# Optimization experiments

Measured on AMD Instinct MI355X. Metric: run time of the kernel, lower is better.

The kernel has to match this reference:

```python
import math
import jax, jax.numpy as jnp
from jax import lax
import numpy as np

N_IMG = 2
C = 128
IMG_H, IMG_W = 512, 1024
STRIDES = (4, 8, 16, 32, 64)
SIZES = (32.0, 64.0, 128.0, 256.0, 512.0)
RATIOS = (0.5, 1.0, 2.0)
A = len(RATIOS)
PRE_NMS_TOPK = 2000    # pre_nms_topk[self.training] with training=True
POST_NMS_TOPK = 1000   # post_nms_topk[self.training]
NMS_THRESH = 0.7
BATCH_PER_IMG = 256
POS_FRAC = 0.5
MIN_BOX_SIZE = 0.0
SCALE_CLAMP = math.log(1000.0 / 16.0)
MATCH_LOW, MATCH_HIGH = 0.3, 0.7


def cell_anchors(size):
    rs = jnp.asarray(RATIOS, jnp.float32)
    area = size * size
    w = jnp.sqrt(area / rs)
    h = w * rs
    return jnp.stack([-w / 2, -h / 2, w / 2, h / 2], axis=1)  # [A,4]


def level_anchors(H, W, stride, size):
    ca = cell_anchors(size)
    sx = jnp.arange(W, dtype=jnp.float32) * stride
    sy = jnp.arange(H, dtype=jnp.float32) * stride
    yy, xx = jnp.meshgrid(sy, sx, indexing="ij")
    shifts = jnp.stack([xx, yy, xx, yy], axis=-1).reshape(-1, 4)  # [H*W,4]
    return (shifts[:, None, :] + ca[None, :, :]).reshape(-1, 4)  # [H*W*A,4]


def pairwise_iou(a, b):
    lt = jnp.maximum(a[:, None, :2], b[None, :, :2])
    rb = jnp.minimum(a[:, None, 2:], b[None, :, 2:])
    wh = jnp.clip(rb - lt, 0.0)
    inter = wh[..., 0] * wh[..., 1]
    area_a = (a[:, 2] - a[:, 0]) * (a[:, 3] - a[:, 1])
    area_b = (b[:, 2] - b[:, 0]) * (b[:, 3] - b[:, 1])
    union = area_a[:, None] + area_b[None, :] - inter
    return jnp.where(inter > 0, inter / union, 0.0)


def get_deltas(src, tgt):
    sw = src[..., 2] - src[..., 0]; sh = src[..., 3] - src[..., 1]
    scx = src[..., 0] + 0.5 * sw;   scy = src[..., 1] + 0.5 * sh
    tw = tgt[..., 2] - tgt[..., 0]; th = tgt[..., 3] - tgt[..., 1]
    tcx = tgt[..., 0] + 0.5 * tw;   tcy = tgt[..., 1] + 0.5 * th
    return jnp.stack([(tcx - scx) / sw, (tcy - scy) / sh,
                      jnp.log(tw / sw), jnp.log(th / sh)], axis=-1)


def apply_deltas(deltas, boxes):
    w = boxes[..., 2] - boxes[..., 0]; h = boxes[..., 3] - boxes[..., 1]
    cx = boxes[..., 0] + 0.5 * w;      cy = boxes[..., 1] + 0.5 * h
    dx, dy = deltas[..., 0], deltas[..., 1]
    dw = jnp.minimum(deltas[..., 2], SCALE_CLAMP)
    dh = jnp.minimum(deltas[..., 3], SCALE_CLAMP)
    pcx = dx * w + cx; pcy = dy * h + cy
    pw = jnp.exp(dw) * w; ph = jnp.exp(dh) * h
    return jnp.stack([pcx - 0.5 * pw, pcy - 0.5 * ph,
                      pcx + 0.5 * pw, pcy + 0.5 * ph], axis=-1)


def conv(x, w, b):
    y = lax.conv_general_dilated(x, w, (1, 1), "SAME",
                                 dimension_numbers=("NCHW", "OIHW", "NCHW"))
    return y + b[None, :, None, None]


def rpn_forward_flat(feats, conv_w, conv_b, obj_w, obj_b, delta_w, delta_b):
    anchors, logits, deltas = [], [], []
    for (stride, size), f in zip(zip(STRIDES, SIZES), feats):
        N, _, H, W = f.shape
        h = jax.nn.relu(conv(f, conv_w, conv_b))
        lg = conv(h, obj_w, obj_b)       # [N,A,H,W]
        dl = conv(h, delta_w, delta_b)   # [N,4A,H,W]
        logits.append(lg.transpose(0, 2, 3, 1).reshape(N, -1))                     # [N,HWA]
        deltas.append(dl.reshape(N, A, 4, H, W).transpose(0, 3, 4, 1, 2).reshape(N, -1, 4))
        anchors.append(level_anchors(H, W, stride, size))
    return anchors, logits, deltas


def label_and_sample(gt_b, key, anchors_all):
    iou = pairwise_iou(gt_b, anchors_all)                 # [G,R]
    matched_idxs = jnp.argmax(iou, axis=0)
    matched_vals = jnp.max(iou, axis=0)
    labels = jnp.where(matched_vals >= MATCH_HIGH, 1,
             jnp.where(matched_vals >= MATCH_LOW, -1, 0))
    highest = jnp.max(iou, axis=1)                        # per-gt best IoU
    lq = jnp.any((iou == highest[:, None]) & (highest[:, None] > 0), axis=0)
    labels = jnp.where(lq, 1, labels)                     # allow_low_quality_matches
    R = labels.shape[0]
    kf, kb = jax.random.split(key)
    fg = labels == 1; bg = labels == 0
    num_fg = jnp.minimum(fg.sum(), int(POS_FRAC * BATCH_PER_IMG))
    num_bg = jnp.minimum(bg.sum(), BATCH_PER_IMG - num_fg)
    def pick(mask, k, num):
        pri = jnp.where(mask, jax.random.uniform(k, (R,)), jnp.inf)
        rank = jnp.argsort(jnp.argsort(pri))
        return rank < num
    sel_fg = pick(fg, kf, num_fg)
    sel_bg = pick(bg, kb, num_bg)
    labels = jnp.where(sel_fg, 1, jnp.where(sel_bg, 0, -1))
    return labels, gt_b[matched_idxs]


def losses_fn(anchors_all, logits_cat, deltas_cat, gt_labels, matched_gt):
    fg = (gt_labels == 1).astype(logits_cat.dtype)          # [N,R]
    gt_deltas = get_deltas(anchors_all[None], matched_gt)   # [N,R,4]
    loc = jnp.sum(jnp.abs(deltas_cat - gt_deltas) * fg[..., None])  # smooth_l1, beta=0
    valid = (gt_labels >= 0).astype(logits_cat.dtype)
    x = logits_cat
    bce = jnp.maximum(x, 0.0) - x * fg + jnp.log1p(jnp.exp(-jnp.abs(x)))
    cls = jnp.sum(bce * valid)
    norm = float(BATCH_PER_IMG) * logits_cat.shape[0]
    return jnp.stack([cls / norm, loc / norm])


def nms_keep(boxes, valid):
    # boxes are sorted by descending score; greedy suppression.
    K = boxes.shape[0]
    iou = pairwise_iou(boxes, boxes)
    idx = jnp.arange(K)
    def body(i, keep):
        sup = (iou[i] > NMS_THRESH) & (idx > i) & keep[i]
        return keep & ~sup
    return lax.fori_loop(0, K, body, valid)


def predict_proposals(anchors, logits, deltas):
    lvl_boxes, lvl_scores = [], []
    for anc, lg, dl in zip(anchors, logits, deltas):
        boxes = apply_deltas(dl, anc[None])             # [N,R_l,4]
        k = min(PRE_NMS_TOPK, lg.shape[1])
        ts, ti = lax.top_k(lg, k)                       # [N,k]
        tb = jnp.take_along_axis(boxes, ti[..., None], axis=1)
        tb = jnp.stack([jnp.clip(tb[..., 0], 0.0, IMG_W), jnp.clip(tb[..., 1], 0.0, IMG_H),
                        jnp.clip(tb[..., 2], 0.0, IMG_W), jnp.clip(tb[..., 3], 0.0, IMG_H)], -1)
        valid = ((tb[..., 2] - tb[..., 0]) > MIN_BOX_SIZE) & ((tb[..., 3] - tb[..., 1]) > MIN_BOX_SIZE)
        keep = jax.vmap(nms_keep)(tb, valid)
        lvl_boxes.append(tb)
        lvl_scores.append(jnp.where(keep, ts, -jnp.inf))
    all_b = jnp.concatenate(lvl_boxes, axis=1)
    all_s = jnp.concatenate(lvl_scores, axis=1)
    fs, fi = lax.top_k(all_s, POST_NMS_TOPK)
    fb = jnp.take_along_axis(all_b, fi[..., None], axis=1)
    return fb, fs


def setup_inputs() -> dict:
    key = jax.random.key(0)
    ks = jax.random.split(key, 12)
    out = {}
    for i, s in enumerate(STRIDES):
        out[f"feat_p{i+2}"] = jax.random.normal(ks[i], (N_IMG, C, IMG_H // s, IMG_W // s), jnp.float32)
    G = 32
    wh_scale = jnp.asarray([IMG_W, IMG_H], jnp.float32)
    cxy = jax.random.uniform(ks[5], (N_IMG, G, 2)) * wh_scale
    wh = 32.0 + jax.random.uniform(ks[6], (N_IMG, G, 2)) * 224.0
    x1y1 = jnp.clip(cxy - wh / 2, 0.0)
    x2y2 = jnp.maximum(jnp.minimum(cxy + wh / 2, wh_scale), x1y1 + 1.0)
    out["gt_boxes"] = jnp.concatenate([x1y1, x2y2], axis=-1)
    out["conv_w"] = 0.01 * jax.random.normal(ks[7], (C, C, 3, 3), jnp.float32)
    out["conv_b"] = jnp.zeros((C,), jnp.float32)
    out["obj_w"] = 0.01 * jax.random.normal(ks[8], (A, C, 1, 1), jnp.float32)
    out["obj_b"] = jnp.zeros((A,), jnp.float32)
    out["delta_w"] = 0.01 * jax.random.normal(ks[9], (4 * A, C, 1, 1), jnp.float32)
    out["delta_b"] = jnp.zeros((4 * A,), jnp.float32)
    return out


def reference(feat_p2, feat_p3, feat_p4, feat_p5, feat_p6, gt_boxes,
              conv_w, conv_b, obj_w, obj_b, delta_w, delta_b):
    feats = [feat_p2, feat_p3, feat_p4, feat_p5, feat_p6]
    anchors, logits, deltas = rpn_forward_flat(feats, conv_w, conv_b, obj_w, obj_b, delta_w, delta_b)
    anchors_all = jnp.concatenate(anchors, axis=0)      # [R,4]
    logits_cat = jnp.concatenate(logits, axis=1)        # [N,R]
    deltas_cat = jnp.concatenate(deltas, axis=1)        # [N,R,4]
    keys = jax.random.split(jax.random.key(42), gt_boxes.shape[0])
    gt_labels, matched_gt = jax.vmap(label_and_sample, in_axes=(0, 0, None))(gt_boxes, keys, anchors_all)
    losses = losses_fn(anchors_all, logits_cat, deltas_cat, gt_labels, matched_gt)
    prop_boxes, prop_scores = predict_proposals(
        anchors,
        [lax.stop_gradient(l) for l in logits],
        [lax.stop_gradient(d) for d in deltas])
    return prop_boxes, prop_scores, losses
```

## Files before the change

kernel.cpp:

```cpp
#include <hip/hip_runtime.h>
#include <stdint.h>
#include <math.h>


#define R_TOT   130944
#define HALF_R  65472
#define TOTK    7920
#define SCALE_CLAMP 4.135166556742356

__host__ __device__ inline void threefry(uint32_t k0, uint32_t k1,
                                         uint32_t x0, uint32_t x1,
                                         uint32_t* o0, uint32_t* o1)
{
  uint32_t ks[3]; ks[0]=k0; ks[1]=k1; ks[2]=k0^k1^0x1BD11BDAu;
  x0 += ks[0]; x1 += ks[1];
  const uint32_t rot0[4] = {13u,15u,26u,6u};
  const uint32_t rot1[4] = {17u,29u,16u,24u};
  for (int i = 0; i < 5; i++){
    const uint32_t* rot = (i & 1) ? rot1 : rot0;
    for (int q = 0; q < 4; q++){
      x0 += x1;
      x1 = (x1 << rot[q]) | (x1 >> (32u - rot[q]));
      x1 ^= x0;
    }
    x0 += ks[(i+1)%3];
    x1 += ks[(i+2)%3] + (uint32_t)(i+1);
  }
  *o0 = x0; *o1 = x1;
}

__device__ inline unsigned long long mono64(double v){
  unsigned long long b = (unsigned long long)__double_as_longlong(v);
  return (b & 0x8000000000000000ull) ? ~b : (b | 0x8000000000000000ull);
}

__device__ __forceinline__ double iou_cf(double g0,double g1,double g2,double g3,
                                         double a0,double a1,double a2,double a3){
  #pragma clang fp contract(off)
  double lt0 = fmax(g0,a0), lt1 = fmax(g1,a1);
  double rb0 = fmin(g2,a2), rb1 = fmin(g3,a3);
  double w = rb0-lt0; if (w<0.0) w=0.0;
  double h = rb1-lt1; if (h<0.0) h=0.0;
  double inter = w*h;
  double aa = (g2-g0)*(g3-g1);
  double ab = (a2-a0)*(a3-a1);
  double uni = aa+ab-inter;
  return inter>0.0 ? inter/uni : 0.0;
}

__device__ __forceinline__ void anchor_of(int r, double* o){
  #pragma clang fp contract(off)
  const int    base[5]={0,98304,122880,129024,130560};
  const int    Wl[5]  ={256,128,64,32,16};
  const double strd[5]={4.0,8.0,16.0,32.0,64.0};
  const double size[5]={32.0,64.0,128.0,256.0,512.0};
  const double ratio[3]={0.5,1.0,2.0};
  int l=0; while (l<4 && r>=base[l+1]) l++;
  int rr=r-base[l]; int pix=rr/3; int a=rr-pix*3;
  int x=pix%Wl[l], y=pix/Wl[l];
  double w=sqrt(size[l]*size[l]/ratio[a]);
  double h=w*ratio[a];
  double sx=(double)x*strd[l], sy=(double)y*strd[l];
  o[0]=sx-0.5*w; o[1]=sy-0.5*h; o[2]=sx+0.5*w; o[3]=sy+0.5*h;
}

__device__ __forceinline__ void decode_box(int ridx, const double* __restrict__ d,
                                           double* __restrict__ o){
  double a[4]; anchor_of(ridx,a);
  double w=a[2]-a[0], h=a[3]-a[1];
  double cx=a[0]+0.5*w, cy=a[1]+0.5*h;
  double dw=fmin(d[2],SCALE_CLAMP), dh=fmin(d[3],SCALE_CLAMP);
  double pcx=d[0]*w+cx, pcy=d[1]*h+cy;
  double pw=exp(dw)*w, ph=exp(dh)*h;
  double x1=pcx-0.5*pw, y1=pcy-0.5*ph;
  double x2=pcx+0.5*pw, y2=pcy+0.5*ph;
  o[0]=fmin(fmax(x1,0.0),1024.0); o[1]=fmin(fmax(y1,0.0),512.0);
  o[2]=fmin(fmax(x2,0.0),1024.0); o[3]=fmin(fmax(y2,0.0),512.0);
}

__device__ inline void bitonic_desc(double* sv, int* si, int M, int tid, int nthr){
  for (int k=2;k<=M;k<<=1)
    for (int j=k>>1;j>0;j>>=1){
      __syncthreads();
      for (int i=tid;i<M;i+=nthr){
        int ixj=i^j;
        if (ixj>i){
          double va=sv[i], vb=sv[ixj]; int ia=si[i], ib=si[ixj];
          bool before = (va>vb) || (va==vb && ia<ib);
          bool up = ((i&k)==0);
          if (up ? !before : before){ sv[i]=vb; sv[ixj]=va; si[i]=ib; si[ixj]=ia; }
        }
      }
    }
  __syncthreads();
}

__device__ inline void bitonic_asc_u(uint32_t* sk, int* si, int M, int tid, int nthr){
  for (int k=2;k<=M;k<<=1)
    for (int j=k>>1;j>0;j>>=1){
      __syncthreads();
      for (int i=tid;i<M;i+=nthr){
        int ixj=i^j;
        if (ixj>i){
          uint32_t ka=sk[i], kb=sk[ixj]; int ia=si[i], ib=si[ixj];
          bool before = (ka<kb) || (ka==kb && ia<ib);
          bool up = ((i&k)==0);
          if (up ? !before : before){ sk[i]=kb; sk[ixj]=ka; si[i]=ib; si[ixj]=ia; }
        }
      }
    }
  __syncthreads();
}

__device__ inline void hist_select(int* hist, int kneed, int tid,
                                   int* shb, int* shk){
  for (int off=1; off<256; off<<=1){
    int v=0;
    if (tid<256 && tid>=off) v=hist[tid-off];
    __syncthreads();
    if (tid<256) hist[tid]+=v;
    __syncthreads();
  }
  if (tid<256){
    int prev = tid ? hist[tid-1] : 0;
    if (prev < kneed && kneed <= hist[tid]){ *shb=tid; *shk=kneed-prev; }
    if (tid==255 && kneed > hist[255]){ *shb=255; *shk=kneed-hist[254]; }
  }
  __syncthreads();
}

__global__ __launch_bounds__(256) void k_pre(const float* __restrict__ cw,
    float* __restrict__ cwTf, const float* __restrict__ gt,
    unsigned long long* __restrict__ highest)
{
  const int bx=blockIdx.x, tid=threadIdx.x;
  if (bx < 576){
    int o = bx*256 + tid;
    if (o >= 147456) return;
    int cc = o & 127; int t = o >> 7;
    int k9 = t % 9;  int ci = t / 9;
    cwTf[(size_t)(ci*9+k9)*128 + cc] = cw[(size_t)cc*1152 + ci*9 + k9];
  } else {
    __shared__ double gts[128];
    __shared__ unsigned long long lmax[32];
    const int gb=bx-576;
    const int img=gb>>6, b=gb&63;
    if (tid<128) gts[tid]=(double)gt[img*128+tid];
    if (tid<32) lmax[tid]=0ull;
    __syncthreads();
    double gm[32];
    #pragma unroll
    for (int g=0;g<32;g++) gm[g]=0.0;
    for (int r=b*256+tid; r<R_TOT; r+=64*256){
      double a[4]; anchor_of(r,a);
      #pragma unroll
      for (int g=0;g<32;g++){
        double v=iou_cf(gts[g*4],gts[g*4+1],gts[g*4+2],gts[g*4+3],a[0],a[1],a[2],a[3]);
        gm[g]=fmax(gm[g],v);
      }
    }
    #pragma unroll
    for (int g=0;g<32;g++){
      double v=gm[g];
      #pragma unroll
      for (int off=1; off<64; off<<=1) v=fmax(v,__shfl_xor(v,off));
      if ((tid&63)==0) atomicMax(&lmax[g],(unsigned long long)__double_as_longlong(v));
    }
    __syncthreads();
    if (tid<32) atomicMax(&highest[img*32+tid], lmax[tid]);
  }
}

#define CTH 4
#define CTW 8

__global__ __launch_bounds__(256,3) void k_conv_label(
    const float* __restrict__ f2, const float* __restrict__ f3,
    const float* __restrict__ f4, const float* __restrict__ f5,
    const float* __restrict__ f6,
    const float* __restrict__ cwTf, const float* __restrict__ cb,
    const float* __restrict__ ow, const float* __restrict__ ob,
    const float* __restrict__ dwt, const float* __restrict__ dbt,
    double* __restrict__ logits, double* __restrict__ dpred,
    const float* __restrict__ gt, const unsigned long long* __restrict__ highest,
    int* __restrict__ prelab, int* __restrict__ matched,
    int* __restrict__ labels, int* __restrict__ counts,
    uint32_t* __restrict__ ub,
    uint32_t kf00,uint32_t kf01,uint32_t kb00,uint32_t kb01,
    uint32_t kf10,uint32_t kf11,uint32_t kb10,uint32_t kb11)
{
  __shared__ double fshd[4][6][12];
  __shared__ __align__(16) char ush[18432];
  float*  wshF = (float*)ush;
  double* hshp = (double*)ush;
  __shared__ float hw[15*128];
  __shared__ float hb[15];

  const int tid=threadIdx.x;
  const int vbid = blockIdx.x;

  if (vbid >= 3752){
    int j = (vbid-3752)*256 + tid;
    if (j >= 2*R_TOT) return;
    int slot = j / HALF_R; int t = j - slot*HALF_R;
    uint32_t k0,k1;
    if      (slot==0){k0=kf00;k1=kf01;}
    else if (slot==1){k0=kb00;k1=kb01;}
    else if (slot==2){k0=kf10;k1=kf11;}
    else             {k0=kb10;k1=kb11;}
    uint32_t o0,o1;
    threefry(k0,k1,(uint32_t)t,(uint32_t)(t+HALF_R),&o0,&o1);
    ub[(size_t)slot*R_TOT+t]=o0;
    ub[(size_t)slot*R_TOT+t+HALF_R]=o1;
    return;
  }

  if (vbid >= 2728){
    double* gts=(double*)ush;
    double* hg =(double*)(ush+1024);
    int* wfg=(int*)(ush+1280); int* wbg=(int*)(ush+1296);
    const int lb=vbid-2728;
    const int img=lb>>9, blk=lb&511;
    if (tid<128) gts[tid]=(double)gt[img*128+tid];
    if (tid<32)  hg[tid]=__longlong_as_double((long long)highest[img*32+tid]);
    __syncthreads();
    int r=blk*256+tid;
    const bool ok=(r<R_TOT);
    int lab=-1, bi=0;
    if (ok){
      double a[4]; anchor_of(r,a);
      double best=-1.0; bool lq=false;
      #pragma unroll
      for (int g=0;g<32;g++){
        double v=iou_cf(gts[g*4],gts[g*4+1],gts[g*4+2],gts[g*4+3],a[0],a[1],a[2],a[3]);
        if (v>best){ best=v; bi=g; }
        if (hg[g]>0.0 && v==hg[g]) lq=true;
      }
      lab = lq ? 1 : (best>=0.7 ? 1 : (best>=0.3 ? -1 : 0));
      prelab [(size_t)img*R_TOT+r]=lab;
      matched[(size_t)img*R_TOT+r]=bi;
      labels [(size_t)img*R_TOT+r]=-1;
    }
    unsigned long long bf=__ballot(ok && lab==1);
    unsigned long long bb=__ballot(ok && lab==0);
    const int wid=tid>>6, lane=tid&63;
    if (lane==0){ wfg[wid]=__popcll(bf); wbg[wid]=__popcll(bb); }
    __syncthreads();
    if (tid==0){
      int fcnt=wfg[0]+wfg[1]+wfg[2]+wfg[3];
      int bcnt=wbg[0]+wbg[1]+wbg[2]+wbg[3];
      if (fcnt) atomicAdd(&counts[img*2+0],fcnt);
      if (bcnt) atomicAdd(&counts[img*2+1],bcnt);
    }
    return;
  }

  const int cumt[6]={0,2048,2560,2688,2720,2728};
  const int Hs[5]={128,64,32,16,8}, Wl[5]={256,128,64,32,16};
  const int rbs[5]={0,98304,122880,129024,130560};
  const int lgx[5]={5,4,3,2,1};

  int bid=vbid;
  int lvl=0;
  while (lvl<4 && bid>=cumt[lvl+1]) lvl++;
  int t=bid-cumt[lvl];
  const int img=t&1; const int tt=t>>1;
  const int H=Hs[lvl], W=Wl[lvl], rbase=rbs[lvl];
  const int tx=tt&((1<<lgx[lvl])-1), ty=tt>>lgx[lvl];
  const int x0=tx*CTW, y0=ty*CTH;
  const float* f = lvl==0?f2: lvl==1?f3: lvl==2?f4: lvl==3?f5: f6;

  for (int i=tid;i<15*128;i+=256){
    int o=i>>7, c=i&127;
    hw[i]=(o<3)?ow[o*128+c]:dwt[(o-3)*128+c];
  }
  if (tid<15) hb[tid]=(tid<3)?ob[tid]:dbt[tid-3];

  const int c=tid&127, half=tid>>7;
  double acc[16];
  #pragma unroll
  for (int i=0;i<16;i++) acc[i]=0.0;

  const float* fimg = f + (size_t)img*128*H*W;

  const bool fin_act = (tid < 240);
  int ci_f=0,dy_f=0,dx_f=0; bool fin_valid=false;
  const float* fptr=fimg;
  if (fin_act){
    ci_f=tid/60; int rem=tid-ci_f*60; dy_f=rem/10; dx_f=rem-dy_f*10;
    int y=y0-1+dy_f, x=x0-1+dx_f;
    fin_valid = (y>=0&&y<H&&x>=0&&x<W);
    fptr = fimg + (size_t)ci_f*H*W + (fin_valid ? ((size_t)y*W+x) : 0);
  }
  const size_t fstep=(size_t)4*H*W;
  const float2* wsrc=(const float2*)cwTf;

  float fin_pf=0.f; float2 wpf[9];
  if (fin_act){ fin_pf = fin_valid ? *fptr : 0.f; fptr += fstep; }
  #pragma unroll
  for (int j2=0;j2<9;j2++) wpf[j2]=wsrc[tid+j2*256];

  for (int ci0=0; ci0<128; ci0+=4){
    __syncthreads();
    if (fin_act) fshd[ci_f][dy_f][dx_f]=(double)fin_pf;
    { float2* wdst=(float2*)wshF;
      #pragma unroll
      for (int j2=0;j2<9;j2++) wdst[tid+j2*256]=wpf[j2]; }
    if (ci0+4<128){
      if (fin_act){ fin_pf = fin_valid ? *fptr : 0.f; fptr += fstep; }
      const float2* wn = wsrc + (size_t)(ci0+4)*576;
      #pragma unroll
      for (int j2=0;j2<9;j2++) wpf[j2]=wn[tid+j2*256];
    }
    __syncthreads();
    #pragma unroll
    for (int ci=0;ci<4;ci++){
      double w9d[9];
      #pragma unroll
      for (int k=0;k<9;k++) w9d[k]=(double)wshF[(ci*9+k)*128 + c];
      #pragma unroll
      for (int irl=0;irl<4;irl++){
        int ir=half*2+irl;
        double rowb[10];
        #pragma unroll
        for (int q=0;q<10;q++) rowb[q]=fshd[ci][ir][q];
        #pragma unroll
        for (int orl=0;orl<2;orl++){
          int ky=irl-orl;
          if (ky<0||ky>2) continue;
          #pragma unroll
          for (int px=0;px<8;px++){
            double s=acc[orl*8+px];
            #pragma unroll
            for (int kx=0;kx<3;kx++) s += w9d[ky*3+kx]*rowb[px+kx];
            acc[orl*8+px]=s;
          }
        }
      }
    }
  }
  double bc=(double)cb[c];
  __syncthreads();
  if (half==0){
    #pragma unroll
    for (int pp=0;pp<16;pp++){
      double hv=acc[pp]+bc; if (hv<0.0) hv=0.0;
      hshp[c*17+pp]=hv;
    }
  }
  __syncthreads();
  for (int hp=0;hp<2;hp++){
    if (tid<240){
      int o=tid>>4, p=tid&15;
      double s=(double)hb[o];
      for (int c2=0;c2<128;c2++) s += (double)hw[o*128+c2]*hshp[c2*17+p];
      int pg=hp*16+p;
      int py=pg>>3, px=pg&7;
      int gy=y0+py, gx=x0+px;
      long long pix=(long long)gy*W+gx;
      size_t rb=(size_t)rbase+(size_t)pix*3;
      if (o<3) logits[(size_t)img*R_TOT+rb+o]=s;
      else { int a=(o-3)>>2, jj=(o-3)&3; dpred[((size_t)img*R_TOT+rb+a)*4+jj]=s; }
    }
    if (hp==0){
      __syncthreads();
      if (half==1){
        #pragma unroll
        for (int pp=0;pp<16;pp++){
          double hv=acc[pp]+bc; if (hv<0.0) hv=0.0;
          hshp[c*17+pp]=hv;
        }
      }
      __syncthreads();
    }
  }
}

__global__ __launch_bounds__(1024) void k_mid2(const uint32_t* __restrict__ ub,
    const int* __restrict__ prelab, const int* __restrict__ counts,
    int* __restrict__ labels,
    const double* __restrict__ logits, const double* __restrict__ dpred,
    double* __restrict__ allS, double* __restrict__ allB,
    unsigned long long* __restrict__ keepbuf)
{
  __shared__ __align__(16) char buf[49152];
  __shared__ int hist[256];
  __shared__ int sI0, sI1;
  __shared__ int cnt;
  const int tid=threadIdx.x;

  if (blockIdx.x < 4){
    uint32_t* skey=(uint32_t*)buf; int* sidx=(int*)(buf+16384);
    const int img=blockIdx.x>>1, cls=blockIdx.x&1;
    const int cfg=counts[img*2+0], cbg=counts[img*2+1];
    const int num_fg=cfg<128?cfg:128;
    const int cap_bg=256-num_fg;
    const int num=cls?(cbg<cap_bg?cbg:cap_bg):num_fg;
    if (num<=0) return;
    const int want=cls?0:1;
    const int sel=want;
    const uint32_t* u=ub+(size_t)(img*2+cls)*R_TOT;
    const int* pl=prelab+(size_t)img*R_TOT;
    int* lab=labels+(size_t)img*R_TOT;

    for (int b=tid;b<256;b+=1024) hist[b]=0;
    if (tid==0) cnt=0;
    __syncthreads();
    #pragma unroll 4
    for (int r=tid;r<R_TOT;r+=1024){
      int plr = pl[r];
      uint32_t key = u[r]>>9;
      if (plr==want) atomicAdd(&hist[key>>15],1);
    }
    __syncthreads();
    hist_select(hist, num, tid, &sI0, &sI1);
    const uint32_t bsel=(uint32_t)sI0; const int kneed=sI1;
    #pragma unroll 4
    for (int r=tid;r<R_TOT;r+=1024){
      int plr = pl[r];
      uint32_t key = u[r]>>9;
      if (plr==want){
        uint32_t t8=key>>15;
        if (t8<bsel) lab[r]=sel;
        else if (t8==bsel){ int p=atomicAdd(&cnt,1); if (p<4096){ skey[p]=key; sidx[p]=r; } }
      }
    }
    __syncthreads();
    int n=cnt<4096?cnt:4096;
    for (int i=tid;i<4096;i+=1024) if (i>=n){ skey[i]=0xFFFFFFFFu; sidx[i]=0x7FFFFFFF; }
    bitonic_asc_u(skey,sidx,4096,tid,1024);
    int take = kneed<n?kneed:n;
    for (int i=tid;i<take;i+=1024) lab[sidx[i]]=sel;
  } else {
    double* sv=(double*)buf; int* si=(int*)(buf+32768);
    const int Rl[5]   ={98304,24576,6144,1536,384};
    const int kl[5]   ={2000,2000,2000,1536,384};
    const int lbase[5]={0,98304,122880,129024,130560};
    const int loff[5] ={0,2000,4000,6000,7536};
    const int bb=blockIdx.x-4;
    const int lvl=bb%5, img=bb/5;
    if (lvl==0 && tid<124) keepbuf[img*124+tid]=~0ull;
    const int Rn=Rl[lvl], K=kl[lvl];
    const double* lg=logits+(size_t)img*R_TOT+lbase[lvl];

    unsigned long long chosen=0; int kneed=K;
    for (int ps=7; ps>=6; --ps){
      int shift=ps*8;
      for (int b=tid;b<256;b+=1024) hist[b]=0;
      __syncthreads();
      #pragma unroll 4
      for (int r=tid;r<Rn;r+=1024){
        unsigned long long ik=~mono64(lg[r]);
        bool okp=(ps==7)||((ik>>(shift+8))==(chosen>>(shift+8)));
        if (okp) atomicAdd(&hist[(int)((ik>>shift)&255)],1);
      }
      __syncthreads();
      hist_select(hist, kneed, tid, &sI0, &sI1);
      chosen = chosen | ((unsigned long long)sI0<<shift);
      kneed  = sI1;
      __syncthreads();
    }
    const unsigned long long lim = chosen | 0xFFFFFFFFFFFFull;
    if (tid==0) cnt=0;
    __syncthreads();
    #pragma unroll 4
    for (int r=tid;r<Rn;r+=1024){
      unsigned long long ik=~mono64(lg[r]);
      if (ik<=lim){ int p=atomicAdd(&cnt,1); if (p<4096){ sv[p]=lg[r]; si[p]=r; } }
    }
    __syncthreads();
    int n=cnt<4096?cnt:4096;
    for (int i=tid;i<4096;i+=1024) if (i>=n){ sv[i]=-HUGE_VAL; si[i]=0x7FFFFFFF; }
    bitonic_desc(sv,si,4096,tid,1024);
    for (int j=tid;j<K;j+=1024){
      double v=sv[j]; int r=si[j];
      size_t slot=(size_t)img*TOTK+loff[lvl]+j;
      allS[slot]=v;
      int ridx=lbase[lvl]+r;
      double bx[4];
      decode_box(ridx, dpred+((size_t)img*R_TOT+ridx)*4, bx);
      allB[slot*4+0]=bx[0]; allB[slot*4+1]=bx[1]; allB[slot*4+2]=bx[2]; allB[slot*4+3]=bx[3];
    }
  }
}

__global__ __launch_bounds__(256) void k_mid3(const double* __restrict__ allB,
    unsigned long long* __restrict__ msk,
    const double* __restrict__ logits, const double* __restrict__ dpred,
    const float* __restrict__ gt, const int* __restrict__ labels,
    const int* __restrict__ matched, double* __restrict__ part)
{
  const int bx=blockIdx.x, tid=threadIdx.x;
  if (bx < 1980){
    __shared__ double Bsh[8000];
    const int kl[5]  ={2000,2000,2000,1536,384};
    const int loff[5]={0,2000,4000,6000,7536};
    const int rbc[6] ={0,250,500,750,942,990};
    const int img = bx/990; int t = bx - img*990;
    int lvl=0; while (lvl<4 && t>=rbc[lvl+1]) lvl++;
    const int i0=(t-rbc[lvl])*8;
    const int K=kl[lvl]; const int nw=(K+63)>>6;
    const double* B=allB+(size_t)(img*TOTK+loff[lvl])*4;
    for (int q=tid;q<K*4;q+=256) Bsh[q]=B[q];
    __syncthreads();
    const int wv=tid>>6, lane=tid&63;
    for (int rr=0;rr<8;rr++){
      int i=i0+rr;
      if (i>=K) break;
      const double bi0=Bsh[i*4],bi1=Bsh[i*4+1],bi2=Bsh[i*4+2],bi3=Bsh[i*4+3];
      const double areai=(bi2-bi0)*(bi3-bi1);
      for (int w=wv;w<nw;w+=4){
        int j=w*64+lane;
        bool pred=false;
        if (j<K && j!=i){
          double a0=Bsh[j*4],a1=Bsh[j*4+1],a2=Bsh[j*4+2],a3=Bsh[j*4+3];
          double lt0=fmax(bi0,a0), lt1=fmax(bi1,a1);
          double rb0=fmin(bi2,a2), rb1=fmin(bi3,a3);
          double ww=rb0-lt0; if (ww<0.0) ww=0.0;
          double hh=rb1-lt1; if (hh<0.0) hh=0.0;
          double inter=ww*hh;
          double uni=areai+(a2-a0)*(a3-a1)-inter;
          double iou=inter>0.0?inter/uni:0.0;
          pred = iou>0.7;
        }
        unsigned long long m=__ballot(pred);
        if (lane==0) msk[((size_t)img*TOTK+loff[lvl]+i)*32+w]=m;
      }
    }
  } else {
    const int bid2=bx-1980;
    double cls=0.0, loc=0.0;
    for (int idx=bid2*256+tid; idx<2*R_TOT; idx+=256*256){
      int l=labels[idx];
      if (l<0) continue;
      double x=logits[idx];
      double fgv=(l==1)?1.0:0.0;
      cls += fmax(x,0.0)-x*fgv+log1p(exp(-fabs(x)));
      if (l==1){
        int img=idx/R_TOT, r=idx-img*R_TOT;
        double a[4]; anchor_of(r,a);
        int m=matched[idx];
        const float* g=gt+img*128+m*4;
        double sw=a[2]-a[0], sh=a[3]-a[1];
        double scx=a[0]+0.5*sw, scy=a[1]+0.5*sh;
        double tw=(double)g[2]-(double)g[0], th=(double)g[3]-(double)g[1];
        double tcx=(double)g[0]+0.5*tw, tcy=(double)g[1]+0.5*th;
        double d0=(tcx-scx)/sw, d1=(tcy-scy)/sh;
        double d2=log(tw/sw), d3=log(th/sh);
        const double* dp=dpred+(size_t)idx*4;
        loc += fabs(dp[0]-d0)+fabs(dp[1]-d1)+fabs(dp[2]-d2)+fabs(dp[3]-d3);
      }
    }
    __shared__ double sc[256], sl[256];
    sc[tid]=cls; sl[tid]=loc; __syncthreads();
    for (int s=128;s>0;s>>=1){
      if (tid<s){ sc[tid]+=sc[tid+s]; sl[tid]+=sl[tid+s]; }
      __syncthreads();
    }
    if (tid==0){ part[bid2*2]=sc[0]; part[bid2*2+1]=sl[0]; }
  }
}

__global__ __launch_bounds__(256) void k_post(const double* __restrict__ allB,
    const double* __restrict__ allS, const unsigned long long* __restrict__ msk,
    const double* __restrict__ part, int* __restrict__ flags,
    unsigned long long* __restrict__ keepbuf, float* __restrict__ out)
{
  const int tid=threadIdx.x, bx=blockIdx.x;
  const int kl[5]  ={2000,2000,2000,1536,384};
  const int loff[5]={0,2000,4000,6000,7536};

  if (bx < 10){
    if (tid >= 64) return;
    const int lvl=bx%5, img=bx/5;
    const int K=kl[lvl], off=loff[lvl], nw=(K+63)>>6;
    const int lane=tid;
    const double* B=allB+(size_t)(img*TOTK+off)*4;
    const unsigned long long* M=msk+((size_t)img*TOTK+off)*32;
    unsigned long long keepw=0ull;
    if (lane<nw){
      for (int b=0;b<64;b++){
        int j=lane*64+b;
        if (j<K){
          double x1=B[(size_t)j*4],y1=B[(size_t)j*4+1],x2=B[(size_t)j*4+2],y2=B[(size_t)j*4+3];
          if ((x2-x1)>0.0 && (y2-y1)>0.0) keepw|=(1ull<<b);
        }
      }
    }
    for (int w=0; w<nw; w++){
      unsigned long long vw = __shfl(keepw, w);
      int row = w*64 + lane;
      unsigned long long mrow = (row<K) ? M[(size_t)row*32+w] : 0ull;
      unsigned long long m_lo = lane ? (mrow & ((1ull<<lane)-1ull)) : 0ull;
      const bool validL = (vw>>lane)&1ull;
      unsigned long long kmask = vw;
      while (true){
        bool s = validL && ((m_lo & kmask)==0ull);
        unsigned long long nk = __ballot(s);
        if (nk==kmask) break;
        kmask = nk;
      }
      if (lane==w) keepw = kmask;
      if (lane>w && lane<nw){
        unsigned long long sup=0ull;
        for (int b=0;b<64;b++){
          if ((kmask>>b)&1ull) sup |= M[(size_t)(w*64+b)*32+lane];
        }
        keepw &= ~sup;
      }
    }
    if (lane<nw){
      int nvalid = K - lane*64; if (nvalid>64) nvalid=64;
      unsigned long long vm = (nvalid>=64) ? ~0ull : ((1ull<<nvalid)-1ull);
      unsigned long long cbits = (~keepw) & vm;
      int gbase = off + lane*64;
      int w0 = gbase>>6, sh = gbase&63;
      unsigned long long* kb = keepbuf + (size_t)img*124;
      if (sh==0){
        if (cbits) atomicAnd(&kb[w0], ~cbits);
      } else {
        unsigned long long lo = cbits << sh;
        unsigned long long hi = cbits >> (64-sh);
        if (lo) atomicAnd(&kb[w0],   ~lo);
        if (hi) atomicAnd(&kb[w0+1], ~hi);
      }
    }
    __threadfence();
    if (tid==0) atomicAdd(&flags[img],1);
    return;
  }

  if (bx < 12){
    const int img=bx-10;
    if (tid==0){
      while (atomicAdd(&flags[img],0) < 5) __builtin_amdgcn_s_sleep(8);
    }
    __syncthreads();
    __threadfence();
    __shared__ unsigned long long kbl[124];
    if (tid<124) kbl[tid]=atomicAdd(&keepbuf[(size_t)img*124+tid],0ull);
    __syncthreads();
    const double* sarr=allS+(size_t)img*TOTK;
    __shared__ int hist[256];
    __shared__ int sI0, sI1;
    __shared__ double sv[4096]; __shared__ int si[4096]; __shared__ int cnt;

    unsigned long long chosen=0; int kneed=1000;
    for (int ps=7; ps>=6; --ps){
      int shift=ps*8;
      hist[tid]=0;
      __syncthreads();
      for (int r=tid;r<TOTK;r+=256){
        bool kept = (kbl[r>>6]>>(r&63))&1ull;
        double val = kept ? sarr[r] : -HUGE_VAL;
        unsigned long long ik=~mono64(val);
        bool okp=(ps==7)||((ik>>(shift+8))==(chosen>>(shift+8)));
        if (okp) atomicAdd(&hist[(int)((ik>>shift)&255)],1);
      }
      __syncthreads();
      hist_select(hist, kneed, tid, &sI0, &sI1);
      chosen = chosen | ((unsigned long long)sI0<<shift);
      kneed  = sI1;
      __syncthreads();
    }
    const unsigned long long lim = chosen | 0xFFFFFFFFFFFFull;
    if (tid==0) cnt=0;
    __syncthreads();
    for (int r=tid;r<TOTK;r+=256){
      bool kept = (kbl[r>>6]>>(r&63))&1ull;
      double val = kept ? sarr[r] : -HUGE_VAL;
      unsigned long long ik=~mono64(val);
      if (ik<=lim){ int p=atomicAdd(&cnt,1); if (p<4096){ sv[p]=val; si[p]=r; } }
    }
    __syncthreads();
    int n=cnt<4096?cnt:4096;
    for (int i=tid;i<4096;i+=256) if (i>=n){ sv[i]=-HUGE_VAL; si[i]=0x7FFFFFFF; }
    bitonic_desc(sv,si,4096,tid,256);
    for (int j=tid;j<1000;j+=256){
      out[8000+img*1000+j]=(float)sv[j];
      int idx=si[j];
      const double* b=allB+((size_t)img*TOTK+idx)*4;
      float* ob=out+((size_t)img*1000+j)*4;
      ob[0]=(float)b[0]; ob[1]=(float)b[1]; ob[2]=(float)b[2]; ob[3]=(float)b[3];
    }
    return;
  }

  __shared__ double sc[256], sl[256];
  sc[tid]=part[tid*2]; sl[tid]=part[tid*2+1];
  __syncthreads();
  for (int s=128;s>0;s>>=1){
    if (tid<s){ sc[tid]+=sc[tid+s]; sl[tid]+=sl[tid+s]; }
    __syncthreads();
  }
  if (tid==0){ out[10000]=(float)(sc[0]/512.0); out[10001]=(float)(sl[0]/512.0); }
}

extern "C" void kernel_launch(void* const* d_in, const int* in_sizes, int n_in,
                              void* d_out, int out_size, void* d_ws, size_t ws_size,
                              hipStream_t stream)
{
  (void)in_sizes; (void)n_in; (void)out_size;
  const float* feats[5];
  for (int i=0;i<5;i++) feats[i]=(const float*)d_in[i];
  const float* gt =(const float*)d_in[5];
  const float* cw =(const float*)d_in[6];
  const float* cb =(const float*)d_in[7];
  const float* ow =(const float*)d_in[8];
  const float* ob =(const float*)d_in[9];
  const float* dwt=(const float*)d_in[10];
  const float* dbt=(const float*)d_in[11];
  float* out=(float*)d_out;

  char* p=(char*)d_ws;
  auto carve=[&](size_t nbytes)->char*{ char* q=p; p += (nbytes+255)&~(size_t)255; return q; };
  double* logits =(double*)carve(2ull*R_TOT*8);
  double* dpred  =(double*)carve(2ull*R_TOT*4*8);
  float* cwTf    =(float*)carve(147456ull*4);
  uint32_t* ub   =(uint32_t*)carve(4ull*R_TOT*4);
  int* prelab    =(int*)carve(2ull*R_TOT*4);
  int* matched   =(int*)carve(2ull*R_TOT*4);
  int* labels    =(int*)carve(2ull*R_TOT*4);
  unsigned long long* highest=(unsigned long long*)carve(2*32*8);
  int* counts    =(int*)carve(256);
  int* flags     =(int*)carve(256);
  double* allS   =(double*)carve(2ull*TOTK*8);
  double* allB   =(double*)carve(2ull*TOTK*4*8);
  unsigned long long* msk=(unsigned long long*)carve(2ull*TOTK*32*8);
  double* part   =(double*)carve(256*2*8);
  unsigned long long* keepbuf=(unsigned long long*)carve(2*124*8);
  if ((size_t)(p-(char*)d_ws) > ws_size) return;

  hipMemsetAsync(highest, 0, 1024, stream);

  uint32_t a0,b0,a1,b1;
  threefry(0u,42u,0u,2u,&a0,&b0);
  threefry(0u,42u,1u,3u,&a1,&b1);
  uint32_t kf00,kf01,kb00,kb01,kf10,kf11,kb10,kb11;
  { uint32_t c0,d0,c1,d1;
    threefry(a0,a1,0u,2u,&c0,&d0); threefry(a0,a1,1u,3u,&c1,&d1);
    kf00=c0; kf01=c1; kb00=d0; kb01=d1;
    threefry(b0,b1,0u,2u,&c0,&d0); threefry(b0,b1,1u,3u,&c1,&d1);
    kf10=c0; kf11=c1; kb10=d0; kb11=d1; }

  k_pre<<<704, 256, 0, stream>>>(cw, cwTf, gt, highest);
  k_conv_label<<<4775, 256, 0, stream>>>(feats[0],feats[1],feats[2],feats[3],feats[4],
      cwTf,cb,ow,ob,dwt,dbt, logits, dpred,
      gt, highest, prelab, matched, labels, counts,
      ub, kf00,kf01,kb00,kb01,kf10,kf11,kb10,kb11);
  k_mid2<<<14, 1024, 0, stream>>>(ub, prelab, counts, labels, logits, dpred, allS, allB, keepbuf);
  k_mid3<<<2236, 256, 0, stream>>>(allB, msk, logits, dpred, gt, labels, matched, part);
  k_post<<<13, 256, 0, stream>>>(allB, allS, msk, part, flags, keepbuf, out);
}
```

Measured before the change: 1.405 ms.

## Fuse NMS mask, loss and post-NMS into one kernel with per-level flags

Merges the IoU-mask/loss kernel and the NMS/top-k post kernel into a single 1024-thread launch. The first blocks spin-wait on per-level atomic counters set by the mask-building blocks, so each level's NMS can start as soon as its own mask rows are done instead of waiting for a full kernel boundary. Mask and loss blocks are regrouped to 1024 threads handling 32 rows each, and the loss reduction now uses 64 partials. This depends on the low-index waiting blocks being scheduled alongside the producer blocks, and a bad schedule could deadlock or leave much of the GPU idle.

```diff
diff --git a/kernel.cpp b/kernel.cpp
--- a/kernel.cpp
+++ b/kernel.cpp
@@ -484,32 +484,182 @@
   }
 }
 
-__global__ __launch_bounds__(256) void k_mid3(const double* __restrict__ allB,
+__global__ __launch_bounds__(1024) void k_mid3post(const double* __restrict__ allB,
     unsigned long long* __restrict__ msk,
     const double* __restrict__ logits, const double* __restrict__ dpred,
     const float* __restrict__ gt, const int* __restrict__ labels,
-    const int* __restrict__ matched, double* __restrict__ part)
+    const int* __restrict__ matched, double* __restrict__ part,
+    const double* __restrict__ allS, int* __restrict__ flags,
+    unsigned long long* __restrict__ keepbuf, float* __restrict__ out)
 {
-  const int bx=blockIdx.x, tid=threadIdx.x;
-  if (bx < 1980){
-    __shared__ double Bsh[8000];
-    const int kl[5]  ={2000,2000,2000,1536,384};
-    const int loff[5]={0,2000,4000,6000,7536};
-    const int rbc[6] ={0,250,500,750,942,990};
-    const int img = bx/990; int t = bx - img*990;
+  __shared__ __align__(16) char ush[64000];
+  const int tid=threadIdx.x, bx=blockIdx.x;
+  const int kl[5]  ={2000,2000,2000,1536,384};
+  const int loff[5]={0,2000,4000,6000,7536};
+  const int MBLK[5]={63,63,63,48,12};
+
+  if (bx < 10){
+    if (tid >= 64) return;
+    const int lvl=bx%5, img=bx/5;
+    const int K=kl[lvl], off=loff[lvl], nw=(K+63)>>6;
+    const int lane=tid;
+    {
+      const int target=MBLK[lvl];
+      while (true){
+        int v = (lane==0) ? atomicAdd(&flags[img*5+lvl],0) : 0;
+        v = __shfl(v,0);
+        if (v>=target) break;
+        __builtin_amdgcn_s_sleep(8);
+      }
+      __threadfence();
+    }
+    const double* B=allB+(size_t)(img*TOTK+off)*4;
+    const unsigned long long* M=msk+((size_t)img*TOTK+off)*32;
+    unsigned long long keepw=0ull;
+    if (lane<nw){
+      for (int b=0;b<64;b++){
+        int j=lane*64+b;
+        if (j<K){
+          double x1=B[(size_t)j*4],y1=B[(size_t)j*4+1],x2=B[(size_t)j*4+2],y2=B[(size_t)j*4+3];
+          if ((x2-x1)>0.0 && (y2-y1)>0.0) keepw|=(1ull<<b);
+        }
+      }
+    }
+    for (int w=0; w<nw; w++){
+      unsigned long long vw = __shfl(keepw, w);
+      int row = w*64 + lane;
+      unsigned long long mrow = (row<K) ? M[(size_t)row*32+w] : 0ull;
+      unsigned long long m_lo = lane ? (mrow & ((1ull<<lane)-1ull)) : 0ull;
+      const bool validL = (vw>>lane)&1ull;
+      unsigned long long kmask = vw;
+      while (true){
+        bool s = validL && ((m_lo & kmask)==0ull);
+        unsigned long long nk = __ballot(s);
+        if (nk==kmask) break;
+        kmask = nk;
+      }
+      if (lane==w) keepw = kmask;
+      if (lane>w && lane<nw){
+        unsigned long long sup=0ull;
+        for (int b=0;b<64;b++){
+          if ((kmask>>b)&1ull) sup |= M[(size_t)(w*64+b)*32+lane];
+        }
+        keepw &= ~sup;
+      }
+    }
+    if (lane<nw){
+      int nvalid = K - lane*64; if (nvalid>64) nvalid=64;
+      unsigned long long vm = (nvalid>=64) ? ~0ull : ((1ull<<nvalid)-1ull);
+      unsigned long long cbits = (~keepw) & vm;
+      int gbase = off + lane*64;
+      int w0 = gbase>>6, sh = gbase&63;
+      unsigned long long* kb = keepbuf + (size_t)img*124;
+      if (sh==0){
+        if (cbits) atomicAnd(&kb[w0], ~cbits);
+      } else {
+        unsigned long long lo = cbits << sh;
+        unsigned long long hi = cbits >> (64-sh);
+        if (lo) atomicAnd(&kb[w0],   ~lo);
+        if (hi) atomicAnd(&kb[w0+1], ~hi);
+      }
+    }
+    __threadfence();
+    if (tid==0) atomicAdd(&flags[10+img],1);
+    return;
+  }
+
+  if (bx < 12){
+    double* sv=(double*)ush;
+    int*    si=(int*)(ush+32768);
+    unsigned long long* kbl=(unsigned long long*)(ush+49152);
+    int*    hist=(int*)(ush+50144);
+    __shared__ int sI0, sI1, cnt;
+    const int img=bx-10;
+    if (tid==0){
+      while (atomicAdd(&flags[10+img],0) < 5) __builtin_amdgcn_s_sleep(8);
+    }
+    __syncthreads();
+    __threadfence();
+    if (tid<124) kbl[tid]=atomicAdd(&keepbuf[(size_t)img*124+tid],0ull);
+    __syncthreads();
+    const double* sarr=allS+(size_t)img*TOTK;
+
+    unsigned long long chosen=0; int kneed=1000;
+    for (int ps=7; ps>=6; --ps){
+      int shift=ps*8;
+      if (tid<256) hist[tid]=0;
+      __syncthreads();
+      for (int r=tid;r<TOTK;r+=1024){
+        bool kept = (kbl[r>>6]>>(r&63))&1ull;
+        double val = kept ? sarr[r] : -HUGE_VAL;
+        unsigned long long ik=~mono64(val);
+        bool okp=(ps==7)||((ik>>(shift+8))==(chosen>>(shift+8)));
+        if (okp) atomicAdd(&hist[(int)((ik>>shift)&255)],1);
+      }
+      __syncthreads();
+      hist_select(hist, kneed, tid, &sI0, &sI1);
+      chosen = chosen | ((unsigned long long)sI0<<shift);
+      kneed  = sI1;
+      __syncthreads();
+    }
+    const unsigned long long lim = chosen | 0xFFFFFFFFFFFFull;
+    if (tid==0) cnt=0;
+    __syncthreads();
+    for (int r=tid;r<TOTK;r+=1024){
+      bool kept = (kbl[r>>6]>>(r&63))&1ull;
+      double val = kept ? sarr[r] : -HUGE_VAL;
+      unsigned long long ik=~mono64(val);
+      if (ik<=lim){ int p=atomicAdd(&cnt,1); if (p<4096){ sv[p]=val; si[p]=r; } }
+    }
+    __syncthreads();
+    int n=cnt<4096?cnt:4096;
+    for (int i=tid;i<4096;i+=1024) if (i>=n){ sv[i]=-HUGE_VAL; si[i]=0x7FFFFFFF; }
+    bitonic_desc(sv,si,4096,tid,1024);
+    for (int j=tid;j<1000;j+=1024){
+      out[8000+img*1000+j]=(float)sv[j];
+      int idx=si[j];
+      const double* b=allB+((size_t)img*TOTK+idx)*4;
+      float* ob=out+((size_t)img*1000+j)*4;
+      ob[0]=(float)b[0]; ob[1]=(float)b[1]; ob[2]=(float)b[2]; ob[3]=(float)b[3];
+    }
+    return;
+  }
+
+  if (bx == 12){
+    double* sc=(double*)ush; double* sl=(double*)(ush+512);
+    if (tid==0){
+      while (atomicAdd(&flags[12],0) < 64) __builtin_amdgcn_s_sleep(8);
+    }
+    __syncthreads();
+    __threadfence();
+    if (tid<64){ sc[tid]=part[tid*2]; sl[tid]=part[tid*2+1]; }
+    __syncthreads();
+    for (int s=32;s>0;s>>=1){
+      if (tid<s){ sc[tid]+=sc[tid+s]; sl[tid]+=sl[tid+s]; }
+      __syncthreads();
+    }
+    if (tid==0){ out[10000]=(float)(sc[0]/512.0); out[10001]=(float)(sl[0]/512.0); }
+    return;
+  }
+
+  if (bx < 511){
+    double* Bsh=(double*)ush;
+    const int rbc[6]={0,63,126,189,237,249};
+    int t = bx-13;
+    const int img = t/249; t -= img*249;
     int lvl=0; while (lvl<4 && t>=rbc[lvl+1]) lvl++;
-    const int i0=(t-rbc[lvl])*8;
+    const int i0=(t-rbc[lvl])*32;
     const int K=kl[lvl]; const int nw=(K+63)>>6;
     const double* B=allB+(size_t)(img*TOTK+loff[lvl])*4;
-    for (int q=tid;q<K*4;q+=256) Bsh[q]=B[q];
+    for (int q=tid;q<K*4;q+=1024) Bsh[q]=B[q];
     __syncthreads();
     const int wv=tid>>6, lane=tid&63;
-    for (int rr=0;rr<8;rr++){
+    for (int rr=0;rr<32;rr++){
       int i=i0+rr;
       if (i>=K) break;
       const double bi0=Bsh[i*4],bi1=Bsh[i*4+1],bi2=Bsh[i*4+2],bi3=Bsh[i*4+3];
       const double areai=(bi2-bi0)*(bi3-bi1);
-      for (int w=wv;w<nw;w+=4){
+      for (int w=wv;w<nw;w+=16){
         int j=w*64+lane;
         bool pred=false;
         if (j<K && j!=i){
@@ -527,10 +677,16 @@
         if (lane==0) msk[((size_t)img*TOTK+loff[lvl]+i)*32+w]=m;
       }
     }
-  } else {
-    const int bid2=bx-1980;
+    __syncthreads();
+    if (tid==0){ __threadfence(); atomicAdd(&flags[img*5+lvl],1); }
+    return;
+  }
+
+  {
+    double* sc=(double*)ush; double* sl=(double*)(ush+8192);
+    const int lb=bx-511;
     double cls=0.0, loc=0.0;
-    for (int idx=bid2*256+tid; idx<2*R_TOT; idx+=256*256){
+    for (int idx=lb*1024+tid; idx<2*R_TOT; idx+=64*1024){
       int l=labels[idx];
       if (l<0) continue;
       double x=logits[idx];
@@ -551,149 +707,17 @@
         loc += fabs(dp[0]-d0)+fabs(dp[1]-d1)+fabs(dp[2]-d2)+fabs(dp[3]-d3);
       }
     }
-    __shared__ double sc[256], sl[256];
     sc[tid]=cls; sl[tid]=loc; __syncthreads();
-    for (int s=128;s>0;s>>=1){
+    for (int s=512;s>0;s>>=1){
       if (tid<s){ sc[tid]+=sc[tid+s]; sl[tid]+=sl[tid+s]; }
       __syncthreads();
     }
-    if (tid==0){ part[bid2*2]=sc[0]; part[bid2*2+1]=sl[0]; }
-  }
-}
-
-__global__ __launch_bounds__(256) void k_post(const double* __restrict__ allB,
-    const double* __restrict__ allS, const unsigned long long* __restrict__ msk,
-    const double* __restrict__ part, int* __restrict__ flags,
-    unsigned long long* __restrict__ keepbuf, float* __restrict__ out)
-{
-  const int tid=threadIdx.x, bx=blockIdx.x;
-  const int kl[5]  ={2000,2000,2000,1536,384};
-  const int loff[5]={0,2000,4000,6000,7536};
-
-  if (bx < 10){
-    if (tid >= 64) return;
-    const int lvl=bx%5, img=bx/5;
-    const int K=kl[lvl], off=loff[lvl], nw=(K+63)>>6;
-    const int lane=tid;
-    const double* B=allB+(size_t)(img*TOTK+off)*4;
-    const unsigned long long* M=msk+((size_t)img*TOTK+off)*32;
-    unsigned long long keepw=0ull;
-    if (lane<nw){
-      for (int b=0;b<64;b++){
-        int j=lane*64+b;
-        if (j<K){
-          double x1=B[(size_t)j*4],y1=B[(size_t)j*4+1],x2=B[(size_t)j*4+2],y2=B[(size_t)j*4+3];
-          if ((x2-x1)>0.0 && (y2-y1)>0.0) keepw|=(1ull<<b);
-        }
-      }
-    }
-    for (int w=0; w<nw; w++){
-      unsigned long long vw = __shfl(keepw, w);
-      int row = w*64 + lane;
-      unsigned long long mrow = (row<K) ? M[(size_t)row*32+w] : 0ull;
-      unsigned long long m_lo = lane ? (mrow & ((1ull<<lane)-1ull)) : 0ull;
-      const bool validL = (vw>>lane)&1ull;
-      unsigned long long kmask = vw;
-      while (true){
-        bool s = validL && ((m_lo & kmask)==0ull);
-        unsigned long long nk = __ballot(s);
-        if (nk==kmask) break;
-        kmask = nk;
-      }
-      if (lane==w) keepw = kmask;
-      if (lane>w && lane<nw){
-        unsigned long long sup=0ull;
-        for (int b=0;b<64;b++){
-          if ((kmask>>b)&1ull) sup |= M[(size_t)(w*64+b)*32+lane];
-        }
-        keepw &= ~sup;
-      }
-    }
-    if (lane<nw){
-      int nvalid = K - lane*64; if (nvalid>64) nvalid=64;
-      unsigned long long vm = (nvalid>=64) ? ~0ull : ((1ull<<nvalid)-1ull);
-      unsigned long long cbits = (~keepw) & vm;
-      int gbase = off + lane*64;
-      int w0 = gbase>>6, sh = gbase&63;
-      unsigned long long* kb = keepbuf + (size_t)img*124;
-      if (sh==0){
-        if (cbits) atomicAnd(&kb[w0], ~cbits);
-      } else {
-        unsigned long long lo = cbits << sh;
-        unsigned long long hi = cbits >> (64-sh);
-        if (lo) atomicAnd(&kb[w0],   ~lo);
-        if (hi) atomicAnd(&kb[w0+1], ~hi);
-      }
-    }
-    __threadfence();
-    if (tid==0) atomicAdd(&flags[img],1);
-    return;
-  }
-
-  if (bx < 12){
-    const int img=bx-10;
     if (tid==0){
-      while (atomicAdd(&flags[img],0) < 5) __builtin_amdgcn_s_sleep(8);
-    }
-    __syncthreads();
-    __threadfence();
-    __shared__ unsigned long long kbl[124];
-    if (tid<124) kbl[tid]=atomicAdd(&keepbuf[(size_t)img*124+tid],0ull);
-    __syncthreads();
-    const double* sarr=allS+(size_t)img*TOTK;
-    __shared__ int hist[256];
-    __shared__ int sI0, sI1;
-    __shared__ double sv[4096]; __shared__ int si[4096]; __shared__ int cnt;
-
-    unsigned long long chosen=0; int kneed=1000;
-    for (int ps=7; ps>=6; --ps){
-      int shift=ps*8;
-      hist[tid]=0;
-      __syncthreads();
-      for (int r=tid;r<TOTK;r+=256){
-        bool kept = (kbl[r>>6]>>(r&63))&1ull;
-        double val = kept ? sarr[r] : -HUGE_VAL;
-        unsigned long long ik=~mono64(val);
-        bool okp=(ps==7)||((ik>>(shift+8))==(chosen>>(shift+8)));
-        if (okp) atomicAdd(&hist[(int)((ik>>shift)&255)],1);
-      }
-      __syncthreads();
-      hist_select(hist, kneed, tid, &sI0, &sI1);
-      chosen = chosen | ((unsigned long long)sI0<<shift);
-      kneed  = sI1;
-      __syncthreads();
-    }
-    const unsigned long long lim = chosen | 0xFFFFFFFFFFFFull;
-    if (tid==0) cnt=0;
-    __syncthreads();
-    for (int r=tid;r<TOTK;r+=256){
-      bool kept = (kbl[r>>6]>>(r&63))&1ull;
-      double val = kept ? sarr[r] : -HUGE_VAL;
-      unsigned long long ik=~mono64(val);
-      if (ik<=lim){ int p=atomicAdd(&cnt,1); if (p<4096){ sv[p]=val; si[p]=r; } }
-    }
-    __syncthreads();
-    int n=cnt<4096?cnt:4096;
-    for (int i=tid;i<4096;i+=256) if (i>=n){ sv[i]=-HUGE_VAL; si[i]=0x7FFFFFFF; }
-    bitonic_desc(sv,si,4096,tid,256);
-    for (int j=tid;j<1000;j+=256){
-      out[8000+img*1000+j]=(float)sv[j];
-      int idx=si[j];
-      const double* b=allB+((size_t)img*TOTK+idx)*4;
-      float* ob=out+((size_t)img*1000+j)*4;
-      ob[0]=(float)b[0]; ob[1]=(float)b[1]; ob[2]=(float)b[2]; ob[3]=(float)b[3];
-    }
-    return;
-  }
-
-  __shared__ double sc[256], sl[256];
-  sc[tid]=part[tid*2]; sl[tid]=part[tid*2+1];
-  __syncthreads();
-  for (int s=128;s>0;s>>=1){
-    if (tid<s){ sc[tid]+=sc[tid+s]; sl[tid]+=sl[tid+s]; }
-    __syncthreads();
-  }
-  if (tid==0){ out[10000]=(float)(sc[0]/512.0); out[10001]=(float)(sl[0]/512.0); }
+      part[lb*2]=sc[0]; part[lb*2+1]=sl[0];
+      __threadfence();
+      atomicAdd(&flags[12],1);
+    }
+  }
 }
 
 extern "C" void kernel_launch(void* const* d_in, const int* in_sizes, int n_in,
@@ -749,6 +773,6 @@
       gt, highest, prelab, matched, labels, counts,
       ub, kf00,kf01,kb00,kb01,kf10,kf11,kb10,kb11);
   k_mid2<<<14, 1024, 0, stream>>>(ub, prelab, counts, labels, logits, dpred, allS, allB, keepbuf);
-  k_mid3<<<2236, 256, 0, stream>>>(allB, msk, logits, dpred, gt, labels, matched, part);
-  k_post<<<13, 256, 0, stream>>>(allB, allS, msk, part, flags, keepbuf, out);
-}
+  k_mid3post<<<575, 1024, 0, stream>>>(allB, msk, logits, dpred, gt, labels, matched,
+      part, allS, flags, keepbuf, out);
+}
```

Result: faster. 1.252 ms (-10.9%).
